# Performance work log

Hardware: AMD Instinct MI355X
Metric: run time of the kernel (lower is better)

The kernel has to match this reference:

```python
import jax, jax.numpy as jnp
import numpy as np


def setup_inputs() -> dict:
    key = jax.random.key(0)
    B, T, F = 1000000, 60, 4
    inputs = jax.random.normal(key, (B, T, F), dtype=jnp.float32)
    return {"inputs": inputs, "window_size": 30, "n_forecast": 14, "target_idx": 0}


def reference(inputs, window_size, n_forecast, target_idx):
    # y: last window_size steps of the target feature -> [B, W]
    y = inputs[:, -window_size:, target_idx]
    W = window_size
    # design points x = 0..W-1 (identical for every sample)
    x = jnp.arange(W, dtype=inputs.dtype)            # [W]
    x_mean = x.mean()
    xc = x - x_mean                                  # centered x, [W]
    sxx = jnp.sum(xc * xc)                           # scalar
    y_mean = y.mean(axis=1)                          # [B]
    # closed-form simple OLS: slope = sum((x-xm)*y)/Sxx (centered y cancels)
    slope = (y @ xc) / sxx                           # [B]
    intercept = y_mean - slope * x_mean              # [B]
    # predict at future timesteps W .. W+n_forecast-1
    t_future = jnp.arange(W, W + n_forecast, dtype=inputs.dtype)  # [n_forecast]
    result = intercept[:, None] + slope[:, None] * t_future[None, :]  # [B, n_forecast]
    return result
```

## Files before the change

### kernel.cpp

```cpp
#include <hip/hip_runtime.h>


#define NBATCH 256
#define W      30
#define NF     14
#define TDIM   60
#define ROWPAD 31

__global__ __launch_bounds__(256)
void linreg_forecast_kernel(const float4* __restrict__ in4,
                            float4* __restrict__ out4,
                            int B, int out4_total)
{
    __shared__ float y[NBATCH * ROWPAD];
    __shared__ float res[NBATCH * NF];

    const int tid = threadIdx.x;
    const int B0  = blockIdx.x * NBATCH;

    #pragma unroll 5
    for (int k = 0; k < W; ++k) {
        int i  = tid + (k << 8);
        int bb = i / W;
        int t  = i - bb * W;
        int gb = B0 + bb;
        if (gb < B) {
            float4 v = in4[gb * TDIM + W + t];
            y[bb * ROWPAD + t] = v.x;
        }
    }
    __syncthreads();

    {
        int gb = B0 + tid;
        if (gb < B) {
            const float* row = &y[tid * ROWPAD];
            float s0 = 0.f, s1 = 0.f;
            #pragma unroll
            for (int t = 0; t < W; ++t) {
                float v = row[t];
                s0 += v;
                s1 += v * ((float)t - 14.5f);
            }
            float slope     = s1 * (1.0f / 2247.5f);
            float intercept = s0 * (1.0f / 30.0f) - slope * 14.5f;
            float* r = &res[tid * NF];
            #pragma unroll
            for (int j = 0; j < NF; ++j)
                r[j] = intercept + slope * (float)(W + j);
        }
    }
    __syncthreads();

    const int base4 = blockIdx.x * (NBATCH * NF / 4);
    #pragma unroll
    for (int k = 0; k < 4; ++k) {
        int i = tid + (k << 8);
        if (i < NBATCH * NF / 4 && base4 + i < out4_total) {
            float4 v;
            v.x = res[4 * i + 0];
            v.y = res[4 * i + 1];
            v.z = res[4 * i + 2];
            v.w = res[4 * i + 3];
            out4[base4 + i] = v;
        }
    }
}

extern "C" void kernel_launch(void* const* d_in, const int* in_sizes, int n_in,
                              void* d_out, int out_size, void* d_ws, size_t ws_size,
                              hipStream_t stream)
{
    const float* in = (const float*)d_in[0];
    float*      out = (float*)d_out;
    int B = in_sizes[0] / (TDIM * 4);
    int grid = (B + NBATCH - 1) / NBATCH;
    linreg_forecast_kernel<<<grid, 256, 0, stream>>>(
        (const float4*)in, (float4*)out, B, out_size / 4);
}
```

Before: 1.151 ms.

## Load window directly into LDS via global_load_lds and reuse buffer for output

Replaces per-thread float4 global loads plus LDS stores with the AMD global_load_lds builtin, which moves each target scalar straight from global memory into shared memory and frees registers. Out-of-range batch indices are clamped instead of branched so the load loop can be fully unrolled. The padded row layout is dropped and the result buffer is aliased onto the input buffer, which halves LDS use and allows vector float4 reads when writing out. Dropping the row padding may add LDS bank conflicts during the per-row reduction, and the extra barrier is needed to make the buffer reuse safe.

```diff
diff --git a/kernel.cpp b/kernel.cpp
--- a/kernel.cpp
+++ b/kernel.cpp
@@ -5,46 +5,51 @@
 #define W      30
 #define NF     14
 #define TDIM   60
-#define ROWPAD 31
+
+typedef const __attribute__((address_space(1))) void gvoid_t;
+typedef __attribute__((address_space(3))) void lvoid_t;
 
 __global__ __launch_bounds__(256)
-void linreg_forecast_kernel(const float4* __restrict__ in4,
+void linreg_forecast_kernel(const float* __restrict__ in,
                             float4* __restrict__ out4,
                             int B, int out4_total)
 {
-    __shared__ float y[NBATCH * ROWPAD];
-    __shared__ float res[NBATCH * NF];
+    __shared__ __align__(16) float y[NBATCH * W];
 
     const int tid = threadIdx.x;
     const int B0  = blockIdx.x * NBATCH;
 
-    #pragma unroll 5
+    #pragma unroll
     for (int k = 0; k < W; ++k) {
         int i  = tid + (k << 8);
         int bb = i / W;
         int t  = i - bb * W;
         int gb = B0 + bb;
-        if (gb < B) {
-            float4 v = in4[gb * TDIM + W + t];
-            y[bb * ROWPAD + t] = v.x;
+        if (gb > B - 1) gb = B - 1;
+        const float* src = in + ((size_t)(gb * TDIM + W + t) << 2);
+        __builtin_amdgcn_global_load_lds((gvoid_t*)src, (lvoid_t*)&y[i], 4, 0, 0);
+    }
+    __syncthreads();
+
+    float slope, intercept;
+    {
+        const float* row = &y[tid * W];
+        float s0 = 0.f, s1 = 0.f;
+        #pragma unroll
+        for (int t = 0; t < W; ++t) {
+            float v = row[t];
+            s0 += v;
+            s1 += v * ((float)t - 14.5f);
         }
+        slope     = s1 * (1.0f / 2247.5f);
+        intercept = s0 * (1.0f / 30.0f) - slope * 14.5f;
     }
     __syncthreads();
 
     {
         int gb = B0 + tid;
         if (gb < B) {
-            const float* row = &y[tid * ROWPAD];
-            float s0 = 0.f, s1 = 0.f;
-            #pragma unroll
-            for (int t = 0; t < W; ++t) {
-                float v = row[t];
-                s0 += v;
-                s1 += v * ((float)t - 14.5f);
-            }
-            float slope     = s1 * (1.0f / 2247.5f);
-            float intercept = s0 * (1.0f / 30.0f) - slope * 14.5f;
-            float* r = &res[tid * NF];
+            float* r = &y[tid * NF];
             #pragma unroll
             for (int j = 0; j < NF; ++j)
                 r[j] = intercept + slope * (float)(W + j);
@@ -53,17 +58,12 @@
     __syncthreads();
 
     const int base4 = blockIdx.x * (NBATCH * NF / 4);
+    const float4* res4 = (const float4*)y;
     #pragma unroll
     for (int k = 0; k < 4; ++k) {
         int i = tid + (k << 8);
-        if (i < NBATCH * NF / 4 && base4 + i < out4_total) {
-            float4 v;
-            v.x = res[4 * i + 0];
-            v.y = res[4 * i + 1];
-            v.z = res[4 * i + 2];
-            v.w = res[4 * i + 3];
-            out4[base4 + i] = v;
-        }
+        if (i < NBATCH * NF / 4 && base4 + i < out4_total)
+            out4[base4 + i] = res4[i];
     }
 }
 
@@ -76,5 +76,5 @@
     int B = in_sizes[0] / (TDIM * 4);
     int grid = (B + NBATCH - 1) / NBATCH;
     linreg_forecast_kernel<<<grid, 256, 0, stream>>>(
-        (const float4*)in, (float4*)out, B, out_size / 4);
+        in, (float4*)out, B, out_size / 4);
 }
```

Result: no change. 1.135 ms (-1.4%).
